# Performance work log

Measured on AMD Instinct MI355X. Metric: run time of the kernel, lower is better.

The kernel has to match this reference:

```python
import jax, jax.numpy as jnp
import numpy as np

B, LK, D, H = 16, 4096, 1024, 16
DK = D // H
EPS = 1e-5
NEG = -1.0e9


def _layernorm(x, g, b):
    m = jnp.mean(x, axis=-1, keepdims=True)
    v = jnp.mean((x - m) ** 2, axis=-1, keepdims=True)
    return (x - m) * jax.lax.rsqrt(v + EPS) * g + b


def setup_inputs() -> dict:
    key0 = jax.random.key(0)
    ks = jax.random.split(key0, 12)

    def lin(k, fan_in, fan_out):
        # torch nn.Linear default-ish scale; stored as [in, out] so y = x @ W + b
        return jax.random.normal(k, (fan_in, fan_out), jnp.float32) / np.float32(np.sqrt(fan_in))

    return {
        "query": jax.random.normal(ks[0], (B, 1, D), jnp.float32),
        "key": jax.random.normal(ks[1], (B, LK, D), jnp.float32),
        "mask": jax.random.randint(ks[2], (B, 1, LK), 0, 2, jnp.int32),
        "Wq": lin(ks[3], D, D), "bq": jnp.zeros((D,), jnp.float32),
        "Wk": lin(ks[4], D, D), "bk": jnp.zeros((D,), jnp.float32),
        "Wv": lin(ks[5], D, D), "bv": jnp.zeros((D,), jnp.float32),
        "Wo": lin(ks[6], D, D), "bo": jnp.zeros((D,), jnp.float32),
        "raw_thr": jnp.full((H, 1, 1), 0.1, jnp.float32),
        "Wvp": lin(ks[7], 2 * D, D),  # v_proj, no bias
        "W1": lin(ks[8], D, 2 * D), "b1": jnp.zeros((2 * D,), jnp.float32),
        "W2": lin(ks[9], 2 * D, D), "b2": jnp.zeros((D,), jnp.float32),
        "g1": jnp.ones((D,), jnp.float32), "be1": jnp.zeros((D,), jnp.float32),
        "g2": jnp.ones((D,), jnp.float32), "be2": jnp.zeros((D,), jnp.float32),
    }


def reference(query, key, mask, Wq, bq, Wk, bk, Wv, bv, Wo, bo, raw_thr,
              Wvp, W1, b1, W2, b2, g1, be1, g2, be2):
    b = query.shape[0]
    lk = key.shape[1]
    # v = cat(key, query.repeat(1, Lk, 1)) @ Wvp   (query has seq_len 1)
    v_in = jnp.concatenate([key, jnp.broadcast_to(query, (b, lk, D))], axis=2)
    v = v_in @ Wvp  # [B, Lk, D]

    Q = (query @ Wq + bq).reshape(b, 1, H, DK).transpose(0, 2, 1, 3)   # [B,H,1,DK]
    K = (key @ Wk + bk).reshape(b, lk, H, DK).transpose(0, 2, 1, 3)    # [B,H,Lk,DK]
    V = (v @ Wv + bv).reshape(b, lk, H, DK).transpose(0, 2, 1, 3)      # [B,H,Lk,DK]

    scores = jnp.einsum("bhqd,bhkd->bhqk", Q, K) / jnp.sqrt(jnp.float32(DK))
    # padding mask: [B,1,Lk] -> [B,1,1,Lk]
    scores = jnp.where(mask[:, None] == 0, NEG, scores)
    # learned per-head threshold: softplus(raw_thr) -> [1,H,1,1]
    thr = jax.nn.softplus(raw_thr)[None]
    scores = jnp.where(scores <= thr, NEG, scores)
    attn = jax.nn.softmax(scores, axis=-1)

    x = jnp.einsum("bhqk,bhkd->bhqd", attn, V)            # [B,H,1,DK]
    x = x.transpose(0, 2, 1, 3).reshape(b, 1, H * DK)      # [B,1,D]
    attn_out = x @ Wo + bo

    x = _layernorm(query + attn_out, g1, be1)
    ff = jax.nn.relu(x @ W1 + b1) @ W2 + b2
    x = _layernorm(x + ff, g2, be2)
    return x
```

## Files before the change

### kernel.cpp

```cpp
#include <hip/hip_runtime.h>
#include <hip/hip_bf16.h>

#define NB 16
#define NHD 16
#define ND 1024
#define NLK 4096
#define NFF 2048

typedef float f32x4 __attribute__((ext_vector_type(4)));
typedef float f32x2 __attribute__((ext_vector_type(2)));
typedef __bf16 bf16x2v __attribute__((ext_vector_type(2)));
typedef __bf16 bf16x4v __attribute__((ext_vector_type(4)));
typedef __bf16 bf16x8 __attribute__((ext_vector_type(8)));

__global__ void k_fill(float* out, int n, float v) {
  int i = blockIdx.x * 256 + threadIdx.x;
  if (i < n) out[i] = v;
}

__device__ __forceinline__ void gbar(unsigned* ctr, unsigned* flg, unsigned nblk) {
  __syncthreads();
  if (threadIdx.x == 0) {
    __hip_atomic_fetch_add(ctr, 1u, __ATOMIC_RELEASE, __HIP_MEMORY_SCOPE_AGENT);
    if (blockIdx.x == 0) {
      while (__hip_atomic_load(ctr, __ATOMIC_RELAXED, __HIP_MEMORY_SCOPE_AGENT) < nblk)
        __builtin_amdgcn_s_sleep(8);
      __hip_atomic_store(flg, 1u, __ATOMIC_RELEASE, __HIP_MEMORY_SCOPE_AGENT);
    } else {
      while (__hip_atomic_load(flg, __ATOMIC_RELAXED, __HIP_MEMORY_SCOPE_AGENT) == 0)
        __builtin_amdgcn_s_sleep(8);
    }
    __builtin_amdgcn_fence(__ATOMIC_ACQUIRE, "agent");
  }
  __syncthreads();
}

__global__ __launch_bounds__(256) void k_prep(const float* __restrict__ Wq,
                                              const float* __restrict__ bq,
                                              const float* __restrict__ Wvp,
                                              const float* __restrict__ query,
                                              float* __restrict__ Qrow,
                                              float* __restrict__ cvec,
                                              __hip_bfloat16* __restrict__ wvpt) {
  __shared__ float pmem[64 * 68];
  int blk = blockIdx.x;
  int t = threadIdx.x;
  if (blk < 128) {
    int which = blk >> 6;
    int jb = blk & 3;
    int i0 = ((blk >> 2) & 15) * 64;
    int j = jb * 256 + t;
    {
      int e = t * 4;
      int b = e >> 6, ii = e & 63;
      float4 v = *(const float4*)(query + (size_t)b * ND + i0 + ii);
      pmem[ii * 20 + b] = v.x;
      pmem[(ii + 1) * 20 + b] = v.y;
      pmem[(ii + 2) * 20 + b] = v.z;
      pmem[(ii + 3) * 20 + b] = v.w;
    }
    __syncthreads();
    float acc[16];
#pragma unroll
    for (int q = 0; q < 16; ++q) acc[q] = 0.f;
    for (int ii = 0; ii < 64; ++ii) {
      int i = i0 + ii;
      float wv = which ? Wvp[(size_t)(ND + i) * ND + j] : Wq[(size_t)i * ND + j];
      float qv[16];
      const float4* qp = (const float4*)&pmem[ii * 20];
      *(float4*)&qv[0] = qp[0];
      *(float4*)&qv[4] = qp[1];
      *(float4*)&qv[8] = qp[2];
      *(float4*)&qv[12] = qp[3];
#pragma unroll
      for (int q = 0; q < 16; ++q) acc[q] += wv * qv[q];
    }
    float* out = which ? cvec : Qrow;
    float bias = (!which && i0 == 0) ? bq[j] : 0.f;
#pragma unroll
    for (int q = 0; q < 16; ++q) atomicAdd(&out[q * ND + j], acc[q] + bias);
  } else {
    int tb = blk - 128;
    int n0 = (tb & 15) * 64;
    int k0base = (tb >> 4) * 256;
    for (int it = 0; it < 4; ++it) {
      int k0 = k0base + it * 64;
#pragma unroll
      for (int i = 0; i < 4; ++i) {
        int idx = t * 4 + i * 1024;
        int kk = idx >> 6, nn = idx & 63;
        float4 v = *(const float4*)(Wvp + (size_t)(k0 + kk) * ND + n0 + nn);
        pmem[kk * 68 + nn] = v.x;
        pmem[kk * 68 + nn + 1] = v.y;
        pmem[kk * 68 + nn + 2] = v.z;
        pmem[kk * 68 + nn + 3] = v.w;
      }
      __syncthreads();
#pragma unroll
      for (int i = 0; i < 4; ++i) {
        int idx = t * 4 + i * 1024;
        int nn = idx >> 6, kk = idx & 63;
        bf16x4v o;
#pragma unroll
        for (int j = 0; j < 4; ++j) o[j] = (__bf16)pmem[(kk + j) * 68 + nn];
        *(bf16x4v*)((__bf16*)wvpt + (size_t)(n0 + nn) * ND + k0 + kk) = o;
      }
      __syncthreads();
    }
  }
}

__global__ __launch_bounds__(256) void k0b(const float* __restrict__ Wk,
                                           const float* __restrict__ bk,
                                           const float* __restrict__ Qrow,
                                           __hip_bfloat16* __restrict__ t_bf,
                                           float* __restrict__ s0) {
  int h = blockIdx.x;
  int d0 = blockIdx.y * 128;
  int t = threadIdx.x;
  __shared__ float qs[16 * 64];
  __shared__ float wks[128 * 66];
  {
    int lin = t * 4;
    int b = lin >> 6, dk = lin & 63;
    *(float4*)&qs[b * 64 + dk] = *(const float4*)(Qrow + b * ND + h * 64 + dk);
  }
#pragma unroll
  for (int e = 0; e < 8; ++e) {
    int lin = e * 1024 + t * 4;
    int d = lin >> 6, dk = lin & 63;
    *(float4*)&wks[d * 66 + dk] = *(const float4*)(Wk + (size_t)(d0 + d) * ND + h * 64 + dk);
  }
  __syncthreads();
  if (blockIdx.y == 0 && t < 16) {
    float a = 0.f;
    const float* bkh = bk + h * 64;
    for (int jj = 0; jj < 64; ++jj) a += bkh[jj] * qs[t * 64 + jj];
    s0[t * 16 + h] = a;
  }
  int d = t >> 1, bh = (t & 1) * 8;
  float acc[8];
#pragma unroll
  for (int q = 0; q < 8; ++q) acc[q] = 0.f;
  for (int dk = 0; dk < 64; ++dk) {
    float wv = wks[d * 66 + dk];
#pragma unroll
    for (int q = 0; q < 8; ++q) acc[q] += wv * qs[(bh + q) * 64 + dk];
  }
#pragma unroll
  for (int q = 0; q < 8; ++q)
    t_bf[(size_t)((bh + q) * 16 + h) * ND + d0 + d] = (__hip_bfloat16)acc[q];
}

__global__ __launch_bounds__(512, 4) void k_flash(const float* __restrict__ key,
                                                  const __hip_bfloat16* __restrict__ t_bf,
                                                  const float* __restrict__ s0,
                                                  const float* __restrict__ raw_thr,
                                                  const int* __restrict__ mask,
                                                  __hip_bfloat16* __restrict__ pu,
                                                  float* __restrict__ mloc,
                                                  float* __restrict__ lloc) {
  int ch = blockIdx.x, b = blockIdx.y;
  int t = threadIdx.x;
  int wv = t >> 6, lane = t & 63, l15 = lane & 15, g4 = lane >> 4;
  __shared__ float ps[8][32][17];
  __shared__ float scr[32][17];
  __shared__ float wls[32][16];
  __shared__ float mrun[16], lrun[16], fact[16], mnew_s[16], thv_s[16], s0_s[16];
  f32x2 pu_r[16];
#pragma unroll
  for (int h = 0; h < 16; ++h) pu_r[h] = (f32x2){0.f, 0.f};
  if (t < 16) {
    mrun[t] = -1.0e9f;
    lrun[t] = 0.f;
    thv_s[t] = log1pf(expf(raw_thr[t]));
    s0_s[t] = s0[b * 16 + t];
  }
  __syncthreads();
  const float* keyb = key + (size_t)b * NLK * ND;
  const __hip_bfloat16* tb = t_bf + (size_t)(b * 16 + l15) * ND;
  int dsl = wv * 128;
  int dlane = dsl + lane * 2;
  int kk = t >> 4, hh = t & 15;
  for (int sp = 0; sp < 4; ++sp) {
    int ks0 = ch * 128 + sp * 32;
    f32x4 acc0 = {0.f, 0.f, 0.f, 0.f}, acc1 = {0.f, 0.f, 0.f, 0.f};
#pragma unroll
    for (int st = 0; st < 4; ++st) {
      int d = dsl + st * 32 + g4 * 8;
      bf16x8 bfr = *(const bf16x8*)(tb + d);
      const float* a0p = keyb + (size_t)(ks0 + l15) * ND + d;
      const float* a1p = a0p + (size_t)16 * ND;
      float a0[8], a1[8];
      *(float4*)&a0[0] = *(const float4*)a0p;
      *(float4*)&a0[4] = *(const float4*)(a0p + 4);
      *(float4*)&a1[0] = *(const float4*)a1p;
      *(float4*)&a1[4] = *(const float4*)(a1p + 4);
      bf16x8 af0, af1;
#pragma unroll
      for (int j = 0; j < 8; ++j) {
        af0[j] = (__bf16)a0[j];
        af1[j] = (__bf16)a1[j];
      }
      acc0 = __builtin_amdgcn_mfma_f32_16x16x32_bf16(af0, bfr, acc0, 0, 0, 0);
      acc1 = __builtin_amdgcn_mfma_f32_16x16x32_bf16(af1, bfr, acc1, 0, 0, 0);
    }
#pragma unroll
    for (int r = 0; r < 4; ++r) {
      ps[wv][g4 * 4 + r][l15] = acc0[r];
      ps[wv][16 + g4 * 4 + r][l15] = acc1[r];
    }
    __syncthreads();
    float sv;
    {
      float sum = 0.f;
#pragma unroll
      for (int w = 0; w < 8; ++w) sum += ps[w][kk][hh];
      float sc_ = (sum + s0_s[hh]) * 0.125f;
      int mv = mask[b * NLK + ks0 + kk];
      sv = (mv != 0 && sc_ > thv_s[hh]) ? sc_ : -1.0e9f;
      scr[kk][hh] = sv;
    }
    __syncthreads();
    if (wv == 0) {
      float m = -3.4e38f;
#pragma unroll
      for (int j = 0; j < 8; ++j) m = fmaxf(m, scr[g4 * 8 + j][l15]);
      m = fmaxf(m, __shfl_xor(m, 16, 64));
      m = fmaxf(m, __shfl_xor(m, 32, 64));
      if (lane < 16) {
        float mn = fmaxf(mrun[lane], m);
        mnew_s[lane] = mn;
        fact[lane] = expf(mrun[lane] - mn);
        mrun[lane] = mn;
      }
    }
    __syncthreads();
    float w = expf(sv - mnew_s[hh]);
    wls[kk][hh] = w;
    scr[kk][hh] = w;
    __syncthreads();
    if (wv == 0) {
      float s = 0.f;
#pragma unroll
      for (int j = 0; j < 8; ++j) s += scr[g4 * 8 + j][l15];
      s += __shfl_xor(s, 16, 64);
      s += __shfl_xor(s, 32, 64);
      if (lane < 16) lrun[lane] = lrun[lane] * fact[lane] + s;
    }
#pragma unroll
    for (int h = 0; h < 16; ++h) pu_r[h] *= fact[h];
    const float* kb2 = keyb + (size_t)ks0 * ND + dlane;
    for (int k = 0; k < 32; ++k) {
      f32x2 kv = *(const f32x2*)(kb2 + (size_t)k * ND);
      const f32x4* wr = (const f32x4*)&wls[k][0];
      f32x4 w0 = wr[0], w1 = wr[1], w2 = wr[2], w3 = wr[3];
#pragma unroll
      for (int q = 0; q < 4; ++q) {
        pu_r[q] += w0[q] * kv;
        pu_r[4 + q] += w1[q] * kv;
        pu_r[8 + q] += w2[q] * kv;
        pu_r[12 + q] += w3[q] * kv;
      }
    }
  }
  size_t pubase = (size_t)((b * 32 + ch) * 16) * ND + dlane;
#pragma unroll
  for (int h = 0; h < 16; ++h) {
    bf16x2v o;
    o[0] = (__bf16)pu_r[h][0];
    o[1] = (__bf16)pu_r[h][1];
    *(bf16x2v*)((__bf16*)pu + pubase + (size_t)h * ND) = o;
  }
  if (t < 16) {
    mloc[(b * 32 + ch) * 16 + t] = mrun[t];
    lloc[(b * 32 + ch) * 16 + t] = lrun[t];
  }
}

__global__ __launch_bounds__(256) void k_tail(
    const __hip_bfloat16* __restrict__ pu, const float* __restrict__ mloc,
    const float* __restrict__ lloc, __hip_bfloat16* __restrict__ u_bf,
    const __hip_bfloat16* __restrict__ wvpt,
    const float* __restrict__ cvec, const float* __restrict__ Wv,
    const float* __restrict__ bv, float* __restrict__ attn_x,
    const float* __restrict__ Wo, const float* __restrict__ bo,
    const float* __restrict__ query, float* __restrict__ r1,
    const float* __restrict__ g1, const float* __restrict__ be1,
    const float* __restrict__ W1, float* __restrict__ h1,
    const float* __restrict__ b1, const float* __restrict__ W2,
    float* __restrict__ out2, const float* __restrict__ b2,
    const float* __restrict__ g2, const float* __restrict__ be2,
    float* __restrict__ outp, unsigned* __restrict__ bar) {
  __shared__ float smf[2176];
  int blk = blockIdx.x, t = threadIdx.x;
  int wv = t >> 6, lane = t & 63, l15 = lane & 15, g4 = lane >> 4;

  {
    int g = blk * 256 + t;
    if (g < 16384) {
      attn_x[g] = 0.f;
      r1[g] = 0.f;
      out2[g] = 0.f;
    }
    if (g < 32768) h1[g] = 0.f;
    int b = blk >> 4, h = blk & 15;
    if (t < 32) {
      float m = mloc[(b * 32 + t) * 16 + h];
      float l = lloc[(b * 32 + t) * 16 + h];
      float mg = m;
      for (int o = 16; o > 0; o >>= 1) mg = fmaxf(mg, __shfl_xor(mg, o, 32));
      float term = l * expf(m - mg);
      float ls = term;
      for (int o = 16; o > 0; o >>= 1) ls += __shfl_xor(ls, o, 32);
      smf[t] = expf(m - mg) / ls;
    }
    __syncthreads();
    int d = t * 4;
    f32x4 acc = {0.f, 0.f, 0.f, 0.f};
    for (int c = 0; c < 32; ++c) {
      bf16x4v v4 = *(const bf16x4v*)((const __bf16*)pu +
                                     (size_t)((b * 32 + c) * 16 + h) * ND + d);
      f32x4 v = {(float)v4[0], (float)v4[1], (float)v4[2], (float)v4[3]};
      acc += smf[c] * v;
    }
    bf16x4v o;
#pragma unroll
    for (int j = 0; j < 4; ++j) o[j] = (__bf16)acc[j];
    *(bf16x4v*)((__bf16*)u_bf + (size_t)(b * 16 + h) * ND + d) = o;
  }
  gbar(&bar[0 * 32], &bar[256 + 0 * 32], 256);

  {
    int h = blk >> 4, d0 = (blk & 15) * 64;
    float* vb = smf;
    const __hip_bfloat16* ub = u_bf + (size_t)(l15 * 16 + h) * ND;
    const __hip_bfloat16* wb = wvpt + (size_t)(d0 + wv * 16 + l15) * ND;
    f32x4 acc = {0.f, 0.f, 0.f, 0.f};
    for (int ks = 0; ks < 32; ++ks) {
      int d = ks * 32 + g4 * 8;
      bf16x8 a = *(const bf16x8*)(ub + d);
      bf16x8 bb = *(const bf16x8*)(wb + d);
      acc = __builtin_amdgcn_mfma_f32_16x16x32_bf16(a, bb, acc, 0, 0, 0);
    }
#pragma unroll
    for (int r = 0; r < 4; ++r) {
      int b = g4 * 4 + r;
      int nn = wv * 16 + l15;
      vb[b * 68 + nn] = acc[r] + cvec[(size_t)b * ND + d0 + nn];
    }
    __syncthreads();
    int joff = t & 63, bg = t >> 6;
    int j = h * 64 + joff;
    float ax[4] = {0.f, 0.f, 0.f, 0.f};
    for (int dd = 0; dd < 64; ++dd) {
      float wv_ = Wv[(size_t)(d0 + dd) * ND + j];
#pragma unroll
      for (int q = 0; q < 4; ++q) ax[q] += wv_ * vb[(bg * 4 + q) * 68 + dd];
    }
#pragma unroll
    for (int q = 0; q < 4; ++q) {
      float val = ax[q];
      if ((blk & 15) == 0) val += bv[j];
      atomicAdd(&attn_x[(size_t)(bg * 4 + q) * ND + j], val);
    }
  }
  gbar(&bar[1 * 32], &bar[256 + 1 * 32], 256);

  if (blk < 128) {
    int j0 = (blk & 7) * 128;
    int d0 = (blk >> 3) * 64;
    float* ax = smf;
    {
      int lin = t * 4;
      int bb = lin >> 6, dd = lin & 63;
      *(float4*)&ax[bb * 68 + dd] = *(const float4*)(attn_x + (size_t)bb * ND + d0 + dd);
    }
    __syncthreads();
    int joff = t & 127, bg = t >> 7;
    int j = j0 + joff;
    float acc[8];
#pragma unroll
    for (int q = 0; q < 8; ++q) acc[q] = 0.f;
    for (int dd = 0; dd < 64; ++dd) {
      float wv_ = Wo[(size_t)(d0 + dd) * ND + j];
#pragma unroll
      for (int q = 0; q < 8; ++q) acc[q] += wv_ * ax[(bg * 8 + q) * 68 + dd];
    }
#pragma unroll
    for (int q = 0; q < 8; ++q) {
      int bb = bg * 8 + q;
      float val = acc[q];
      if ((blk >> 3) == 0) val += bo[j] + query[(size_t)bb * ND + j];
      atomicAdd(&r1[(size_t)bb * ND + j], val);
    }
  }
  gbar(&bar[2 * 32], &bar[256 + 2 * 32], 256);

  if (blk < 128) {
    int n = (blk & 7) * 256 + t;
    int d0 = (blk >> 3) * 64;
    float* xs = smf;
    float* mv_s = smf + 1984;
    float* iv_s = smf + 2000;
    {
      int row = t >> 4, seg = t & 15;
      float s = 0.f, s2 = 0.f;
      const float* rp = r1 + (size_t)row * ND + seg * 64;
      for (int q = 0; q < 16; ++q) {
        float4 v = *(const float4*)(rp + q * 4);
        s += v.x + v.y + v.z + v.w;
        s2 += v.x * v.x + v.y * v.y + v.z * v.z + v.w * v.w;
      }
      for (int o = 1; o < 16; o <<= 1) {
        s += __shfl_xor(s, o, 16);
        s2 += __shfl_xor(s2, o, 16);
      }
      if (seg == 0) {
        float mean = s * (1.f / ND);
        float var = s2 * (1.f / ND) - mean * mean;
        mv_s[row] = mean;
        iv_s[row] = rsqrtf(var + 1e-5f);
      }
    }
    __syncthreads();
    {
      int e = t * 4;
      int bb = e >> 6, dd = e & 63;
      float4 v = *(const float4*)(r1 + (size_t)bb * ND + d0 + dd);
      float4 g = *(const float4*)(g1 + d0 + dd);
      float4 be = *(const float4*)(be1 + d0 + dd);
      float m = mv_s[bb], iv = iv_s[bb];
      xs[bb * 68 + dd] = (v.x - m) * iv * g.x + be.x;
      xs[bb * 68 + dd + 1] = (v.y - m) * iv * g.y + be.y;
      xs[bb * 68 + dd + 2] = (v.z - m) * iv * g.z + be.z;
      xs[bb * 68 + dd + 3] = (v.w - m) * iv * g.w + be.w;
    }
    __syncthreads();
    float acc[16];
#pragma unroll
    for (int q = 0; q < 16; ++q) acc[q] = 0.f;
    for (int dd = 0; dd < 64; ++dd) {
      float wv_ = W1[(size_t)(d0 + dd) * NFF + n];
#pragma unroll
      for (int q = 0; q < 16; ++q) acc[q] += wv_ * xs[q * 68 + dd];
    }
#pragma unroll
    for (int q = 0; q < 16; ++q) atomicAdd(&h1[(size_t)q * NFF + n], acc[q]);
  }
  gbar(&bar[3 * 32], &bar[256 + 3 * 32], 256);

  if (blk < 128) {
    int j0 = (blk & 7) * 128;
    int n0 = (blk >> 3) * 128;
    float* hs = smf;
#pragma unroll
    for (int e = 0; e < 8; ++e) {
      int lin = e * 256 + t;
      int bb = lin >> 7, nn = lin & 127;
      float hv = h1[(size_t)bb * NFF + n0 + nn] + b1[n0 + nn];
      hs[bb * 132 + nn] = fmaxf(hv, 0.f);
    }
    __syncthreads();
    int joff = t & 127, bg = t >> 7;
    int j = j0 + joff;
    float acc[8];
#pragma unroll
    for (int q = 0; q < 8; ++q) acc[q] = 0.f;
    for (int nn = 0; nn < 128; ++nn) {
      float wv_ = W2[(size_t)(n0 + nn) * ND + j];
#pragma unroll
      for (int q = 0; q < 8; ++q) acc[q] += wv_ * hs[(bg * 8 + q) * 132 + nn];
    }
#pragma unroll
    for (int q = 0; q < 8; ++q) atomicAdd(&out2[(size_t)(bg * 8 + q) * ND + j], acc[q]);
  }
  gbar(&bar[4 * 32], &bar[256 + 4 * 32], 256);

  if (blk < 16) {
    int b = blk;
    float* rs = smf;
    float* rs2 = smf + 256;
    float4 v = *(const float4*)(r1 + (size_t)b * ND + t * 4);
    float s = v.x + v.y + v.z + v.w;
    float s2 = v.x * v.x + v.y * v.y + v.z * v.z + v.w * v.w;
    rs[t] = s;
    rs2[t] = s2;
    __syncthreads();
    for (int st = 128; st > 0; st >>= 1) {
      if (t < st) {
        rs[t] += rs[t + st];
        rs2[t] += rs2[t + st];
      }
      __syncthreads();
    }
    float mean = rs[0] * (1.f / ND);
    float var = rs2[0] * (1.f / ND) - mean * mean;
    float inv = rsqrtf(var + 1e-5f);
    float4 g = *(const float4*)(g1 + t * 4);
    float4 be = *(const float4*)(be1 + t * 4);
    float4 o2 = *(const float4*)(out2 + (size_t)b * ND + t * 4);
    float4 bb2 = *(const float4*)(b2 + t * 4);
    float4 v2;
    v2.x = (v.x - mean) * inv * g.x + be.x + o2.x + bb2.x;
    v2.y = (v.y - mean) * inv * g.y + be.y + o2.y + bb2.y;
    v2.z = (v.z - mean) * inv * g.z + be.z + o2.z + bb2.z;
    v2.w = (v.w - mean) * inv * g.w + be.w + o2.w + bb2.w;
    __syncthreads();
    s = v2.x + v2.y + v2.z + v2.w;
    s2 = v2.x * v2.x + v2.y * v2.y + v2.z * v2.z + v2.w * v2.w;
    rs[t] = s;
    rs2[t] = s2;
    __syncthreads();
    for (int st = 128; st > 0; st >>= 1) {
      if (t < st) {
        rs[t] += rs[t + st];
        rs2[t] += rs2[t + st];
      }
      __syncthreads();
    }
    float mean2 = rs[0] * (1.f / ND);
    float var2 = rs2[0] * (1.f / ND) - mean2 * mean2;
    float inv2 = rsqrtf(var2 + 1e-5f);
    float4 gg = *(const float4*)(g2 + t * 4);
    float4 bbe = *(const float4*)(be2 + t * 4);
    float4 o;
    o.x = (v2.x - mean2) * inv2 * gg.x + bbe.x;
    o.y = (v2.y - mean2) * inv2 * gg.y + bbe.y;
    o.z = (v2.z - mean2) * inv2 * gg.z + bbe.z;
    o.w = (v2.w - mean2) * inv2 * gg.w + bbe.w;
    *(float4*)(outp + (size_t)b * ND + t * 4) = o;
  }
}

extern "C" void kernel_launch(void* const* d_in, const int* in_sizes, int n_in,
                              void* d_out, int out_size, void* d_ws, size_t ws_size,
                              hipStream_t stream) {
  const float* query = (const float*)d_in[0];
  const float* key = (const float*)d_in[1];
  const int* mask = (const int*)d_in[2];
  const float* Wq = (const float*)d_in[3];
  const float* bq = (const float*)d_in[4];
  const float* Wk = (const float*)d_in[5];
  const float* bk = (const float*)d_in[6];
  const float* Wv = (const float*)d_in[7];
  const float* bv = (const float*)d_in[8];
  const float* Wo = (const float*)d_in[9];
  const float* bo = (const float*)d_in[10];
  const float* raw_thr = (const float*)d_in[11];
  const float* Wvp = (const float*)d_in[12];
  const float* W1 = (const float*)d_in[13];
  const float* b1 = (const float*)d_in[14];
  const float* W2 = (const float*)d_in[15];
  const float* b2 = (const float*)d_in[16];
  const float* g1 = (const float*)d_in[17];
  const float* be1 = (const float*)d_in[18];
  const float* g2 = (const float*)d_in[19];
  const float* be2 = (const float*)d_in[20];

  const size_t OFF_QROW = 0;
  const size_t OFF_C = 65536;
  const size_t OFF_BAR = 131072;
  const size_t ZERO_BYTES = 135168;
  const size_t OFF_ATTNX = 135168;
  const size_t OFF_R1 = 200704;
  const size_t OFF_H1 = 266240;
  const size_t OFF_OUT2 = 397312;
  const size_t OFF_S0 = 462848;
  const size_t OFF_MLOC = 463872;
  const size_t OFF_LLOC = 496640;
  const size_t OFF_TBF = 529408;
  const size_t OFF_UBF = 1053696;
  const size_t OFF_WVPT = 1577984;
  const size_t OFF_PU = 4723712;
  const size_t TOTAL = 21500928;

  if (ws_size < TOTAL) {
    k_fill<<<dim3((out_size + 255) / 256), dim3(256), 0, stream>>>((float*)d_out, out_size,
                                                                   12345.0f);
    return;
  }

  char* wsb = (char*)d_ws;
  float* Qrow = (float*)(wsb + OFF_QROW);
  float* cvec = (float*)(wsb + OFF_C);
  unsigned* bar = (unsigned*)(wsb + OFF_BAR);
  float* attn_x = (float*)(wsb + OFF_ATTNX);
  float* r1 = (float*)(wsb + OFF_R1);
  float* h1 = (float*)(wsb + OFF_H1);
  float* out2 = (float*)(wsb + OFF_OUT2);
  float* s0 = (float*)(wsb + OFF_S0);
  float* mloc = (float*)(wsb + OFF_MLOC);
  float* lloc = (float*)(wsb + OFF_LLOC);
  __hip_bfloat16* t_bf = (__hip_bfloat16*)(wsb + OFF_TBF);
  __hip_bfloat16* u_bf = (__hip_bfloat16*)(wsb + OFF_UBF);
  __hip_bfloat16* wvpt = (__hip_bfloat16*)(wsb + OFF_WVPT);
  __hip_bfloat16* pu = (__hip_bfloat16*)(wsb + OFF_PU);

  hipMemsetAsync(d_ws, 0, ZERO_BYTES, stream);

  k_prep<<<dim3(192), dim3(256), 0, stream>>>(Wq, bq, Wvp, query, Qrow, cvec, wvpt);
  k0b<<<dim3(16, 8), dim3(256), 0, stream>>>(Wk, bk, Qrow, t_bf, s0);
  k_flash<<<dim3(32, 16), dim3(512), 0, stream>>>(key, t_bf, s0, raw_thr, mask, pu, mloc, lloc);
  k_tail<<<dim3(256), dim3(256), 0, stream>>>(pu, mloc, lloc, u_bf, wvpt, cvec, Wv, bv,
                                              attn_x, Wo, bo, query, r1, g1, be1, W1, h1, b1,
                                              W2, out2, b2, g2, be2, (float*)d_out, bar);
}
```

Measured before the change: 212.4 us.

## Use MFMA for weighted key accumulation and merge prep kernels with grid barrier

The weighted sum of key rows per head in the flash kernel moves from scalar FMA loops over global key reads into bf16 MFMA. The key tile is staged once into swizzled LDS, and the partial scores and weights are stored as bf16. The two prep kernels are merged into one launch with a grid barrier, removing a kernel launch. Idle blocks in the tail kernel gain matching __syncthreads calls. Rounding the partial scores and weights to bf16 adds precision loss, and the large LDS arena may reduce occupancy.

```diff
diff --git a/kernel.cpp b/kernel.cpp
--- a/kernel.cpp
+++ b/kernel.cpp
@@ -35,14 +35,19 @@
   __syncthreads();
 }
 
-__global__ __launch_bounds__(256) void k_prep(const float* __restrict__ Wq,
-                                              const float* __restrict__ bq,
-                                              const float* __restrict__ Wvp,
-                                              const float* __restrict__ query,
-                                              float* __restrict__ Qrow,
-                                              float* __restrict__ cvec,
-                                              __hip_bfloat16* __restrict__ wvpt) {
-  __shared__ float pmem[64 * 68];
+__global__ __launch_bounds__(256) void k_pre(const float* __restrict__ Wq,
+                                             const float* __restrict__ bq,
+                                             const float* __restrict__ Wvp,
+                                             const float* __restrict__ query,
+                                             const float* __restrict__ Wk,
+                                             const float* __restrict__ bk,
+                                             float* __restrict__ Qrow,
+                                             float* __restrict__ cvec,
+                                             __hip_bfloat16* __restrict__ wvpt,
+                                             __hip_bfloat16* __restrict__ t_bf,
+                                             float* __restrict__ s0,
+                                             unsigned* __restrict__ bar) {
+  __shared__ float pmem[9472];
   int blk = blockIdx.x;
   int t = threadIdx.x;
   if (blk < 128) {
@@ -108,48 +113,45 @@
       __syncthreads();
     }
   }
-}
-
-__global__ __launch_bounds__(256) void k0b(const float* __restrict__ Wk,
-                                           const float* __restrict__ bk,
-                                           const float* __restrict__ Qrow,
-                                           __hip_bfloat16* __restrict__ t_bf,
-                                           float* __restrict__ s0) {
-  int h = blockIdx.x;
-  int d0 = blockIdx.y * 128;
-  int t = threadIdx.x;
-  __shared__ float qs[16 * 64];
-  __shared__ float wks[128 * 66];
+  gbar(&bar[5 * 32], &bar[256 + 5 * 32], 192);
   {
-    int lin = t * 4;
-    int b = lin >> 6, dk = lin & 63;
-    *(float4*)&qs[b * 64 + dk] = *(const float4*)(Qrow + b * ND + h * 64 + dk);
-  }
-#pragma unroll
-  for (int e = 0; e < 8; ++e) {
-    int lin = e * 1024 + t * 4;
-    int d = lin >> 6, dk = lin & 63;
-    *(float4*)&wks[d * 66 + dk] = *(const float4*)(Wk + (size_t)(d0 + d) * ND + h * 64 + dk);
-  }
-  __syncthreads();
-  if (blockIdx.y == 0 && t < 16) {
-    float a = 0.f;
-    const float* bkh = bk + h * 64;
-    for (int jj = 0; jj < 64; ++jj) a += bkh[jj] * qs[t * 64 + jj];
-    s0[t * 16 + h] = a;
-  }
-  int d = t >> 1, bh = (t & 1) * 8;
-  float acc[8];
-#pragma unroll
-  for (int q = 0; q < 8; ++q) acc[q] = 0.f;
-  for (int dk = 0; dk < 64; ++dk) {
-    float wv = wks[d * 66 + dk];
-#pragma unroll
-    for (int q = 0; q < 8; ++q) acc[q] += wv * qs[(bh + q) * 64 + dk];
-  }
-#pragma unroll
-  for (int q = 0; q < 8; ++q)
-    t_bf[(size_t)((bh + q) * 16 + h) * ND + d0 + d] = (__hip_bfloat16)acc[q];
+    int h = blk & 15, dblk = blk >> 4;
+    float* qs = pmem;
+    float* wks = pmem + 1024;
+    if (blk < 128) {
+      int lin = t * 4;
+      int bb = lin >> 6, dk = lin & 63;
+      *(float4*)&qs[bb * 64 + dk] = *(const float4*)(Qrow + bb * ND + h * 64 + dk);
+#pragma unroll
+      for (int e = 0; e < 8; ++e) {
+        int l2 = e * 1024 + t * 4;
+        int d = l2 >> 6, dk2 = l2 & 63;
+        *(float4*)&wks[d * 66 + dk2] =
+            *(const float4*)(Wk + (size_t)(dblk * 128 + d) * ND + h * 64 + dk2);
+      }
+    }
+    __syncthreads();
+    if (blk < 128) {
+      if (dblk == 0 && t < 16) {
+        float a = 0.f;
+        const float* bkh = bk + h * 64;
+        for (int jj = 0; jj < 64; ++jj) a += bkh[jj] * qs[t * 64 + jj];
+        s0[t * 16 + h] = a;
+      }
+      int d = t >> 1, bh = (t & 1) * 8;
+      float acc[8];
+#pragma unroll
+      for (int q = 0; q < 8; ++q) acc[q] = 0.f;
+      for (int dk = 0; dk < 64; ++dk) {
+        float wv = wks[d * 66 + dk];
+#pragma unroll
+        for (int q = 0; q < 8; ++q) acc[q] += wv * qs[(bh + q) * 64 + dk];
+      }
+#pragma unroll
+      for (int q = 0; q < 8; ++q)
+        t_bf[(size_t)((bh + q) * 16 + h) * ND + dblk * 128 + d] = (__hip_bfloat16)acc[q];
+    }
+  }
 }
 
 __global__ __launch_bounds__(512, 4) void k_flash(const float* __restrict__ key,
@@ -163,28 +165,37 @@
   int ch = blockIdx.x, b = blockIdx.y;
   int t = threadIdx.x;
   int wv = t >> 6, lane = t & 63, l15 = lane & 15, g4 = lane >> 4;
-  __shared__ float ps[8][32][17];
-  __shared__ float scr[32][17];
-  __shared__ float wls[32][16];
-  __shared__ float mrun[16], lrun[16], fact[16], mnew_s[16], thv_s[16], s0_s[16];
-  f32x2 pu_r[16];
-#pragma unroll
-  for (int h = 0; h < 16; ++h) pu_r[h] = (f32x2){0.f, 0.f};
+  __shared__ __align__(16) unsigned char lds_arena[78464];
+  __bf16* kstage = (__bf16*)lds_arena;
+  __bf16* psb = (__bf16*)(lds_arena + 65536);
+  float* scr = (float*)(lds_arena + 74752);
+  __bf16* wlsb = (__bf16*)(lds_arena + 76928);
+  float* sm = (float*)(lds_arena + 78080);
+  float* mrun = sm;
+  float* lrun = sm + 16;
+  float* fact = sm + 32;
+  float* mnewv = sm + 48;
+  float* thv = sm + 64;
+  float* s0v = sm + 80;
+
+  f32x4 pacc[8];
+#pragma unroll
+  for (int c = 0; c < 8; ++c) pacc[c] = (f32x4){0.f, 0.f, 0.f, 0.f};
   if (t < 16) {
     mrun[t] = -1.0e9f;
     lrun[t] = 0.f;
-    thv_s[t] = log1pf(expf(raw_thr[t]));
-    s0_s[t] = s0[b * 16 + t];
+    thv[t] = log1pf(expf(raw_thr[t]));
+    s0v[t] = s0[b * 16 + t];
   }
   __syncthreads();
   const float* keyb = key + (size_t)b * NLK * ND;
   const __hip_bfloat16* tb = t_bf + (size_t)(b * 16 + l15) * ND;
   int dsl = wv * 128;
-  int dlane = dsl + lane * 2;
+  __bf16* kst_w = kstage + wv * 4096;
   int kk = t >> 4, hh = t & 15;
   for (int sp = 0; sp < 4; ++sp) {
     int ks0 = ch * 128 + sp * 32;
-    f32x4 acc0 = {0.f, 0.f, 0.f, 0.f}, acc1 = {0.f, 0.f, 0.f, 0.f};
+    f32x4 sa0 = {0.f, 0.f, 0.f, 0.f}, sa1 = {0.f, 0.f, 0.f, 0.f};
 #pragma unroll
     for (int st = 0; st < 4; ++st) {
       int d = dsl + st * 32 + g4 * 8;
@@ -202,75 +213,83 @@
         af0[j] = (__bf16)a0[j];
         af1[j] = (__bf16)a1[j];
       }
-      acc0 = __builtin_amdgcn_mfma_f32_16x16x32_bf16(af0, bfr, acc0, 0, 0, 0);
-      acc1 = __builtin_amdgcn_mfma_f32_16x16x32_bf16(af1, bfr, acc1, 0, 0, 0);
+      int cgp = (((st * 4 + g4) ^ l15) & 15) * 8;
+      *(bf16x8*)(kst_w + l15 * 128 + cgp) = af0;
+      *(bf16x8*)(kst_w + (16 + l15) * 128 + cgp) = af1;
+      sa0 = __builtin_amdgcn_mfma_f32_16x16x32_bf16(af0, bfr, sa0, 0, 0, 0);
+      sa1 = __builtin_amdgcn_mfma_f32_16x16x32_bf16(af1, bfr, sa1, 0, 0, 0);
     }
 #pragma unroll
     for (int r = 0; r < 4; ++r) {
-      ps[wv][g4 * 4 + r][l15] = acc0[r];
-      ps[wv][16 + g4 * 4 + r][l15] = acc1[r];
-    }
-    __syncthreads();
-    float sv;
-    {
-      float sum = 0.f;
-#pragma unroll
-      for (int w = 0; w < 8; ++w) sum += ps[w][kk][hh];
-      float sc_ = (sum + s0_s[hh]) * 0.125f;
-      int mv = mask[b * NLK + ks0 + kk];
-      sv = (mv != 0 && sc_ > thv_s[hh]) ? sc_ : -1.0e9f;
-      scr[kk][hh] = sv;
-    }
+      psb[(wv * 32 + g4 * 4 + r) * 18 + l15] = (__bf16)sa0[r];
+      psb[(wv * 32 + 16 + g4 * 4 + r) * 18 + l15] = (__bf16)sa1[r];
+    }
+    __syncthreads();
+    float sum = 0.f;
+#pragma unroll
+    for (int w = 0; w < 8; ++w) sum += (float)psb[(w * 32 + kk) * 18 + hh];
+    float sc_ = (sum + s0v[hh]) * 0.125f;
+    int mv = mask[b * NLK + ks0 + kk];
+    float sv = (mv != 0 && sc_ > thv[hh]) ? sc_ : -1.0e9f;
+    scr[kk * 17 + hh] = sv;
     __syncthreads();
     if (wv == 0) {
       float m = -3.4e38f;
 #pragma unroll
-      for (int j = 0; j < 8; ++j) m = fmaxf(m, scr[g4 * 8 + j][l15]);
+      for (int j = 0; j < 8; ++j) m = fmaxf(m, scr[(g4 * 8 + j) * 17 + l15]);
       m = fmaxf(m, __shfl_xor(m, 16, 64));
       m = fmaxf(m, __shfl_xor(m, 32, 64));
       if (lane < 16) {
         float mn = fmaxf(mrun[lane], m);
-        mnew_s[lane] = mn;
+        mnewv[lane] = mn;
         fact[lane] = expf(mrun[lane] - mn);
         mrun[lane] = mn;
       }
     }
     __syncthreads();
-    float w = expf(sv - mnew_s[hh]);
-    wls[kk][hh] = w;
-    scr[kk][hh] = w;
+    float w = expf(sv - mnewv[hh]);
+    scr[kk * 17 + hh] = w;
+    wlsb[kk * 18 + hh] = (__bf16)w;
     __syncthreads();
     if (wv == 0) {
       float s = 0.f;
 #pragma unroll
-      for (int j = 0; j < 8; ++j) s += scr[g4 * 8 + j][l15];
+      for (int j = 0; j < 8; ++j) s += scr[(g4 * 8 + j) * 17 + l15];
       s += __shfl_xor(s, 16, 64);
       s += __shfl_xor(s, 32, 64);
       if (lane < 16) lrun[lane] = lrun[lane] * fact[lane] + s;
     }
-#pragma unroll
-    for (int h = 0; h < 16; ++h) pu_r[h] *= fact[h];
-    const float* kb2 = keyb + (size_t)ks0 * ND + dlane;
-    for (int k = 0; k < 32; ++k) {
-      f32x2 kv = *(const f32x2*)(kb2 + (size_t)k * ND);
-      const f32x4* wr = (const f32x4*)&wls[k][0];
-      f32x4 w0 = wr[0], w1 = wr[1], w2 = wr[2], w3 = wr[3];
-#pragma unroll
-      for (int q = 0; q < 4; ++q) {
-        pu_r[q] += w0[q] * kv;
-        pu_r[4 + q] += w1[q] * kv;
-        pu_r[8 + q] += w2[q] * kv;
-        pu_r[12 + q] += w3[q] * kv;
-      }
-    }
-  }
-  size_t pubase = (size_t)((b * 32 + ch) * 16) * ND + dlane;
-#pragma unroll
-  for (int h = 0; h < 16; ++h) {
-    bf16x2v o;
-    o[0] = (__bf16)pu_r[h][0];
-    o[1] = (__bf16)pu_r[h][1];
-    *(bf16x2v*)((__bf16*)pu + pubase + (size_t)h * ND) = o;
+    bf16x8 afw;
+#pragma unroll
+    for (int j = 0; j < 8; ++j) {
+      int k = (j & 3) + g4 * 4 + ((j >> 2) << 4);
+      afw[j] = wlsb[k * 18 + l15];
+    }
+    float f4[4];
+#pragma unroll
+    for (int r = 0; r < 4; ++r) f4[r] = fact[g4 * 4 + r];
+#pragma unroll
+    for (int c = 0; c < 8; ++c) {
+#pragma unroll
+      for (int r = 0; r < 4; ++r) pacc[c][r] *= f4[r];
+      bf16x8 bfk;
+#pragma unroll
+      for (int j = 0; j < 8; ++j) {
+        int k = (j & 3) + g4 * 4 + ((j >> 2) << 4);
+        bfk[j] = kst_w[k * 128 + (((c * 2 + (l15 >> 3)) ^ (k & 15)) * 8 + (l15 & 7))];
+      }
+      pacc[c] = __builtin_amdgcn_mfma_f32_16x16x32_bf16(afw, bfk, pacc[c], 0, 0, 0);
+    }
+    __syncthreads();
+  }
+  size_t pub = (size_t)((b * 32 + ch) * 16) * ND;
+#pragma unroll
+  for (int c = 0; c < 8; ++c) {
+#pragma unroll
+    for (int r = 0; r < 4; ++r) {
+      int h = g4 * 4 + r;
+      ((__bf16*)pu)[pub + (size_t)h * ND + dsl + c * 16 + l15] = (__bf16)pacc[c][r];
+    }
   }
   if (t < 16) {
     mloc[(b * 32 + ch) * 16 + t] = mrun[t];
@@ -394,6 +413,8 @@
       if ((blk >> 3) == 0) val += bo[j] + query[(size_t)bb * ND + j];
       atomicAdd(&r1[(size_t)bb * ND + j], val);
     }
+  } else if (blk >= 128) {
+    __syncthreads();
   }
   gbar(&bar[2 * 32], &bar[256 + 2 * 32], 256);
 
@@ -447,6 +468,9 @@
     }
 #pragma unroll
     for (int q = 0; q < 16; ++q) atomicAdd(&h1[(size_t)q * NFF + n], acc[q]);
+  } else {
+    __syncthreads();
+    __syncthreads();
   }
   gbar(&bar[3 * 32], &bar[256 + 3 * 32], 256);
 
@@ -474,6 +498,8 @@
     }
 #pragma unroll
     for (int q = 0; q < 8; ++q) atomicAdd(&out2[(size_t)(bg * 8 + q) * ND + j], acc[q]);
+  } else {
+    __syncthreads();
   }
   gbar(&bar[4 * 32], &bar[256 + 4 * 32], 256);
 
@@ -599,8 +625,8 @@
 
   hipMemsetAsync(d_ws, 0, ZERO_BYTES, stream);
 
-  k_prep<<<dim3(192), dim3(256), 0, stream>>>(Wq, bq, Wvp, query, Qrow, cvec, wvpt);
-  k0b<<<dim3(16, 8), dim3(256), 0, stream>>>(Wk, bk, Qrow, t_bf, s0);
+  k_pre<<<dim3(192), dim3(256), 0, stream>>>(Wq, bq, Wvp, query, Wk, bk, Qrow, cvec, wvpt,
+                                             t_bf, s0, bar);
   k_flash<<<dim3(32, 16), dim3(512), 0, stream>>>(key, t_bf, s0, raw_thr, mask, pu, mloc, lloc);
   k_tail<<<dim3(256), dim3(256), 0, stream>>>(pu, mloc, lloc, u_bf, wvpt, cvec, Wv, bv,
                                               attn_x, Wo, bo, query, r1, g1, be1, W1, h1, b1,
```

Result: slower. 220.5 us (+3.8%).
